# Kernel optimization log

Measured on AMD Instinct MI355X. Metric: run time of the kernel, lower is better.

The kernel has to match this reference:

```python
import jax, jax.numpy as jnp
import numpy as np

PAD = 1
THRESH = 10.0


def setup_inputs() -> dict:
    key = jax.random.key(0)
    k1, k2, k3 = jax.random.split(key, 3)
    x = jax.random.normal(k1, (8, 16, 62, 62), dtype=jnp.float32)
    W = jax.random.normal(k2, (32, 16, 3, 3), dtype=jnp.float32)
    b = jax.random.normal(k3, (32,), dtype=jnp.float32)
    return {"x": x, "W": W, "b": b}


def reference(x, W, b):
    # ZeroPad2d(padding) on all four sides
    x = jnp.pad(x, ((0, 0), (0, 0), (PAD, PAD), (PAD, PAD)))
    T, C, xr, xc = x.shape
    O, _, wr, wc = W.shape
    L = xr * xc

    # get_xfft_thresh: 1D FFT over flattened HxW, zero coeffs with |Re| < thresh
    xf = jnp.fft.fft(x.reshape(T, C, L))                      # (T,C,L) complex
    xf = jnp.where(jnp.abs(xf.real) < THRESH, jnp.zeros_like(xf), xf)

    # get_Wfft: zero-pad kernel to (xr,xc) bottom/right, flatten, reverse along
    # length (flipud(flip([0,1])) nets to a flip of the last axis only), then FFT
    Wp = jnp.pad(W, ((0, 0), (0, 0), (0, xr - wr), (0, xc - wc))).reshape(O, C, L)
    Wf = jnp.fft.fft(Wp[:, :, ::-1])                          # (O,C,L) complex

    # fftConv1D, batched over (image, out_channel):
    y = jnp.fft.ifft(xf[:, None, :, :] * Wf[None, :, :, :]).real  # (T,O,C,L)
    # torch.roll(y, 1) with no dims rolls the FLATTENED (C*L) tensor by 1
    y = jnp.roll(y.reshape(T, O, C * L), 1, axis=-1).reshape(T, O, C, xr, xc)
    y = y.sum(axis=2)                                         # sum over in-channels
    ans_r, ans_c = xr - wr + 1, xc - wc + 1
    y = y[:, :, :ans_r, :ans_c]
    return y + b[None, :, None, None]
```

## Files before the change

kernel.cpp:

```cpp
#include <hip/hip_runtime.h>
#include <math.h>

#define TWO_PI 6.28318530717958647692f
#define NT     512
#define RPW    8
#define PITCH  65
#define THRESH 10.0f
#define C64    0.995184726672196886f
#define S64    0.098017140329560602f
#define C4096  0.999998823451701879f
#define S4096  0.001533980186284766f

__device__ __forceinline__ int brev6(int x) {
    return (int)(__brev((unsigned)x) >> 26);
}

__device__ __forceinline__ void fft64_dif(float (&re)[RPW], float (&im)[RPW],
                                          int lane, float sign) {
    #pragma unroll
    for (int h = 32; h >= 1; h >>= 1) {
        int j = lane & (h - 1);
        float ang = sign * (TWO_PI / 64.0f) * (float)(j * (32 / h));
        float wr, wi;
        __sincosf(ang, &wi, &wr);
        bool upper = (lane & h) != 0;
        float cwr = upper ? wr : 1.0f;
        float cwi = upper ? wi : 0.0f;
        float sgn = upper ? -1.0f : 1.0f;
        #pragma unroll
        for (int m = 0; m < RPW; ++m) {
            float orr = __shfl_xor(re[m], h, 64);
            float oii = __shfl_xor(im[m], h, 64);
            float ar = fmaf(sgn, re[m], orr);
            float ai = fmaf(sgn, im[m], oii);
            re[m] = ar * cwr - ai * cwi;
            im[m] = ar * cwi + ai * cwr;
        }
    }
}

__device__ __forceinline__ void fft64_dit(float (&re)[RPW], float (&im)[RPW],
                                          int lane, float sign) {
    #pragma unroll
    for (int h = 1; h <= 32; h <<= 1) {
        int j = lane & (h - 1);
        float ang = sign * (TWO_PI / 64.0f) * (float)(j * (32 / h));
        float wr, wi;
        __sincosf(ang, &wi, &wr);
        bool upper = (lane & h) != 0;
        float cwr = upper ? wr : 1.0f;
        float cwi = upper ? wi : 0.0f;
        float sgn = upper ? -1.0f : 1.0f;
        #pragma unroll
        for (int m = 0; m < RPW; ++m) {
            float tr = re[m] * cwr - im[m] * cwi;
            float ti = re[m] * cwi + im[m] * cwr;
            float orr = __shfl_xor(tr, h, 64);
            float oii = __shfl_xor(ti, h, 64);
            re[m] = fmaf(sgn, tr, orr);
            im[m] = fmaf(sgn, ti, oii);
        }
    }
}

__global__ __launch_bounds__(NT) void fwd_kernel(const float* __restrict__ x,
                                                 float2* __restrict__ X) {
    __shared__ float sre[64 * PITCH];
    __shared__ float sim[64 * PITCH];
    const int tc   = blockIdx.x;
    const int tid  = threadIdx.x;
    const int lane = tid & 63;
    const int w    = tid >> 6;
    const float* xrow = x + (size_t)tc * 62 * 62;

    for (int idx = tid; idx < 4096; idx += NT) {
        int r = idx >> 6, s = idx & 63;
        float v = 0.0f;
        if (r >= 1 && r <= 62 && s >= 1 && s <= 62)
            v = xrow[(r - 1) * 62 + (s - 1)];
        sre[r * PITCH + s] = v;
    }
    __syncthreads();

    float re[RPW], im[RPW];
    #pragma unroll
    for (int m = 0; m < RPW; ++m) {
        re[m] = sre[lane * PITCH + (w * RPW + m)];
        im[m] = 0.0f;
    }
    fft64_dif(re, im, lane, -1.0f);
    const int k1 = brev6(lane);
    {
        float cr, ci, sr, si;
        __sincosf(-(TWO_PI / 512.0f) * (float)(k1 * w), &ci, &cr);
        __sincosf(-(TWO_PI / 4096.0f) * (float)k1, &si, &sr);
        #pragma unroll
        for (int m = 0; m < RPW; ++m) {
            float rr = re[m] * cr - im[m] * ci;
            im[m]    = re[m] * ci + im[m] * cr;
            re[m]    = rr;
            float nr = cr * sr - ci * si;
            ci = cr * si + ci * sr; cr = nr;
        }
    }
    __syncthreads();
    #pragma unroll
    for (int m = 0; m < RPW; ++m) {
        int n2 = w * RPW + m;
        sre[k1 * PITCH + n2] = re[m];
        sim[k1 * PITCH + n2] = im[m];
    }
    __syncthreads();
    #pragma unroll
    for (int m = 0; m < RPW; ++m) {
        int row = w * RPW + m;
        re[m] = sre[row * PITCH + lane];
        im[m] = sim[row * PITCH + lane];
    }
    fft64_dif(re, im, lane, -1.0f);
    float2* Xrow = X + (size_t)tc * 4096;
    #pragma unroll
    for (int m = 0; m < RPW; ++m) {
        int row = w * RPW + m;
        float rr = re[m], ii = im[m];
        if (fabsf(rr) < THRESH) { rr = 0.0f; ii = 0.0f; }
        Xrow[row * 64 + lane] = make_float2(rr, ii);
    }
}

__global__ __launch_bounds__(NT, 4) void conv_kernel(const float2* __restrict__ X,
                                                     const float* __restrict__ W,
                                                     const float* __restrict__ b,
                                                     float* __restrict__ out) {
    __shared__ float sre[64 * PITCH];
    __shared__ float sim[64 * PITCH];
    __shared__ __align__(16) float Wsh[16 * 12];
    const int t    = blockIdx.x >> 5;
    const int o    = blockIdx.x & 31;
    const int tid  = threadIdx.x;
    const int lane = tid & 63;
    const int w    = tid >> 6;
    if (tid < 144) {
        int c = tid / 9, q = tid - c * 9;
        Wsh[c * 12 + q] = W[o * 144 + tid];
    }
    __syncthreads();

    const int k2 = brev6(lane);
    float elr, eli;
    __sincosf((TWO_PI / 64.0f) * (float)k2, &eli, &elr);

    float ur[RPW], ui[RPW], vr[RPW], vi[RPW], v2r[RPW], v2i[RPW];
    {
        float cur, cui, cvr, cvi;
        __sincosf((TWO_PI / 8.0f) * (float)w, &cui, &cur);
        __sincosf((TWO_PI / 512.0f) * (float)w, &cvi, &cvr);
        #pragma unroll
        for (int m = 0; m < RPW; ++m) {
            ur[m] = cur; ui[m] = cui;
            float vvr = cvr * elr - cvi * eli;
            float vvi = cvr * eli + cvi * elr;
            vr[m] = vvr; vi[m] = vvi;
            v2r[m] = vvr * vvr - vvi * vvi;
            v2i[m] = 2.0f * vvr * vvi;
            float nur = cur * C64 - cui * S64;
            cui = cur * S64 + cui * C64; cur = nur;
            float nvr = cvr * C4096 - cvi * S4096;
            cvi = cvr * S4096 + cvi * C4096; cvr = nvr;
        }
    }

    float Sr[RPW], Si[RPW];
    #pragma unroll
    for (int m = 0; m < RPW; ++m) { Sr[m] = 0.0f; Si[m] = 0.0f; }

    const float2* Xt = X + (size_t)t * 16 * 4096 + (w * (RPW * 64) + lane);
    #pragma unroll 1
    for (int c = 0; c < 16; ++c) {
        const float4* wp = (const float4*)&Wsh[c * 12];
        float4 wa = wp[0];
        float4 wb = wp[1];
        float  w8 = wp[2].x;
        const float2* xp = Xt + c * 4096;
        #pragma unroll
        for (int m = 0; m < RPW; ++m) {
            float2 xv = xp[m * 64];
            float h0r = fmaf(v2r[m], wa.z, fmaf(vr[m], wa.y, wa.x));
            float h0i = fmaf(v2i[m], wa.z, vi[m] * wa.y);
            float h1r = fmaf(v2r[m], wb.y, fmaf(vr[m], wb.x, wa.w));
            float h1i = fmaf(v2i[m], wb.y, vi[m] * wb.x);
            float h2r = fmaf(v2r[m], w8, fmaf(vr[m], wb.w, wb.z));
            float h2i = fmaf(v2i[m], w8, vi[m] * wb.w);
            float inr = fmaf(ur[m], h2r, fmaf(-ui[m], h2i, h1r));
            float ini = fmaf(ur[m], h2i, fmaf( ui[m], h2r, h1i));
            float Pr  = fmaf(ur[m], inr, fmaf(-ui[m], ini, h0r));
            float Pi  = fmaf(ur[m], ini, fmaf( ui[m], inr, h0i));
            Sr[m] = fmaf(xv.x, Pr, fmaf(-xv.y, Pi, Sr[m]));
            Si[m] = fmaf(xv.x, Pi, fmaf( xv.y, Pr, Si[m]));
        }
    }

    float re[RPW], im[RPW];
    #pragma unroll
    for (int m = 0; m < RPW; ++m) { re[m] = Sr[m]; im[m] = Si[m]; }
    fft64_dit(re, im, lane, +1.0f);
    {
        float cr, ci, sr, si;
        __sincosf((TWO_PI / 512.0f) * (float)(lane * w), &ci, &cr);
        __sincosf((TWO_PI / 4096.0f) * (float)lane, &si, &sr);
        #pragma unroll
        for (int m = 0; m < RPW; ++m) {
            float rr = re[m] * cr - im[m] * ci;
            im[m]    = re[m] * ci + im[m] * cr;
            re[m]    = rr;
            float nr = cr * sr - ci * si;
            ci = cr * si + ci * sr; cr = nr;
        }
    }
    #pragma unroll
    for (int m = 0; m < RPW; ++m) {
        int k1 = w * RPW + m;
        sre[k1 * PITCH + lane] = re[m];
        sim[k1 * PITCH + lane] = im[m];
    }
    __syncthreads();
    #pragma unroll
    for (int m = 0; m < RPW; ++m) {
        int n2 = w * RPW + m;
        re[m] = sre[lane * PITCH + n2];
        im[m] = sim[lane * PITCH + n2];
    }
    fft64_dif(re, im, lane, +1.0f);
    __syncthreads();
    const int n1 = brev6(lane);
    #pragma unroll
    for (int m = 0; m < RPW; ++m) {
        int n2 = w * RPW + m;
        sre[n1 * PITCH + n2] = re[m];
    }
    __syncthreads();
    const float bias = b[o];
    float* orow = out + (size_t)blockIdx.x * 62 * 62;
    for (int idx = tid; idx < 62 * 62; idx += NT) {
        int r = idx / 62, s = idx - r * 62;
        orow[idx] = sre[r * PITCH + s] * (1.0f / 4096.0f) + bias;
    }
}

extern "C" void kernel_launch(void* const* d_in, const int* in_sizes, int n_in,
                              void* d_out, int out_size, void* d_ws, size_t ws_size,
                              hipStream_t stream) {
    const float* x = (const float*)d_in[0];
    const float* W = (const float*)d_in[1];
    const float* b = (const float*)d_in[2];
    float* out = (float*)d_out;
    float2* X = (float2*)d_ws;

    fwd_kernel<<<dim3(128), dim3(NT), 0, stream>>>(x, X);
    conv_kernel<<<dim3(256), dim3(NT), 0, stream>>>(X, W, b, out);
}
```

Baseline: 91.15 us.

## Split forward FFT into two half-sized kernels and pipeline conv channel loads

The forward 4096-point FFT becomes two kernels, each launched with 256 blocks that handle half the data. The intermediate result goes through a global workspace, which doubles block-level parallelism on the GPU. The conv kernel now uses packed 2-float vector math, reads weights directly from global memory instead of staging them in shared memory, and software-prefetches the next channel's spectrum while computing the current one. Launch bounds drop from 4 to 2 waves per EU to allow more registers. The costs are an extra kernel launch, a global round-trip for the intermediate data, and possibly lower occupancy.

```diff
diff --git a/kernel.cpp b/kernel.cpp
--- a/kernel.cpp
+++ b/kernel.cpp
@@ -11,11 +11,20 @@
 #define C4096  0.999998823451701879f
 #define S4096  0.001533980186284766f
 
+typedef float v2f __attribute__((ext_vector_type(2)));
+
 __device__ __forceinline__ int brev6(int x) {
     return (int)(__brev((unsigned)x) >> 26);
 }
 
-__device__ __forceinline__ void fft64_dif(float (&re)[RPW], float (&im)[RPW],
+__device__ __forceinline__ v2f cmul_add(v2f a, v2f b, v2f acc) {
+    acc += (v2f){a.x, a.x} * b;
+    acc += (v2f){a.y, a.y} * (v2f){-b.y, b.x};
+    return acc;
+}
+
+template<int R>
+__device__ __forceinline__ void fft64_dif(float (&re)[R], float (&im)[R],
                                           int lane, float sign) {
     #pragma unroll
     for (int h = 32; h >= 1; h >>= 1) {
@@ -28,7 +37,7 @@
         float cwi = upper ? wi : 0.0f;
         float sgn = upper ? -1.0f : 1.0f;
         #pragma unroll
-        for (int m = 0; m < RPW; ++m) {
+        for (int m = 0; m < R; ++m) {
             float orr = __shfl_xor(re[m], h, 64);
             float oii = __shfl_xor(im[m], h, 64);
             float ar = fmaf(sgn, re[m], orr);
@@ -39,7 +48,8 @@
     }
 }
 
-__device__ __forceinline__ void fft64_dit(float (&re)[RPW], float (&im)[RPW],
+template<int R>
+__device__ __forceinline__ void fft64_dit(float (&re)[R], float (&im)[R],
                                           int lane, float sign) {
     #pragma unroll
     for (int h = 1; h <= 32; h <<= 1) {
@@ -52,7 +62,7 @@
         float cwi = upper ? wi : 0.0f;
         float sgn = upper ? -1.0f : 1.0f;
         #pragma unroll
-        for (int m = 0; m < RPW; ++m) {
+        for (int m = 0; m < R; ++m) {
             float tr = re[m] * cwr - im[m] * cwi;
             float ti = re[m] * cwi + im[m] * cwr;
             float orr = __shfl_xor(tr, h, 64);
@@ -63,37 +73,159 @@
     }
 }
 
-__global__ __launch_bounds__(NT) void fwd_kernel(const float* __restrict__ x,
-                                                 float2* __restrict__ X) {
-    __shared__ float sre[64 * PITCH];
-    __shared__ float sim[64 * PITCH];
-    const int tc   = blockIdx.x;
+__global__ __launch_bounds__(NT) void fwdA_kernel(const float* __restrict__ x,
+                                                  float2* __restrict__ Xa) {
+    __shared__ float sre[64 * 33];
+    __shared__ float sim[64 * 33];
+    const int task = blockIdx.x >> 1;
+    const int h    = blockIdx.x & 1;
     const int tid  = threadIdx.x;
     const int lane = tid & 63;
     const int w    = tid >> 6;
-    const float* xrow = x + (size_t)tc * 62 * 62;
-
-    for (int idx = tid; idx < 4096; idx += NT) {
-        int r = idx >> 6, s = idx & 63;
+    const float* xr = x + (size_t)task * 62 * 62;
+    for (int idx = tid; idx < 64 * 32; idx += NT) {
+        int r = idx >> 5, j = idx & 31;
+        int n2 = 32 * h + j;
         float v = 0.0f;
-        if (r >= 1 && r <= 62 && s >= 1 && s <= 62)
-            v = xrow[(r - 1) * 62 + (s - 1)];
-        sre[r * PITCH + s] = v;
-    }
-    __syncthreads();
+        if (r >= 1 && r <= 62 && n2 >= 1 && n2 <= 62)
+            v = xr[(r - 1) * 62 + (n2 - 1)];
+        sre[r * 33 + j] = v;
+    }
+    __syncthreads();
+    float re[4], im[4];
+    #pragma unroll
+    for (int m = 0; m < 4; ++m) {
+        re[m] = sre[lane * 33 + (w * 4 + m)];
+        im[m] = 0.0f;
+    }
+    fft64_dif<4>(re, im, lane, -1.0f);
+    __syncthreads();
+    const int k1 = brev6(lane);
+    #pragma unroll
+    for (int m = 0; m < 4; ++m) {
+        int j  = w * 4 + m;
+        int n2 = 32 * h + j;
+        float cr, ci;
+        __sincosf(-(TWO_PI / 4096.0f) * (float)(k1 * n2), &ci, &cr);
+        sre[k1 * 33 + j] = re[m] * cr - im[m] * ci;
+        sim[k1 * 33 + j] = re[m] * ci + im[m] * cr;
+    }
+    __syncthreads();
+    float2* Arow = Xa + (size_t)task * 4096;
+    for (int idx = tid; idx < 64 * 32; idx += NT) {
+        int k = idx >> 5, j = idx & 31;
+        Arow[k * 64 + 32 * h + j] = make_float2(sre[k * 33 + j], sim[k * 33 + j]);
+    }
+}
+
+__global__ __launch_bounds__(NT) void fwdB_kernel(const float2* __restrict__ Xa,
+                                                  float2* __restrict__ X) {
+    const int task = blockIdx.x >> 1;
+    const int h    = blockIdx.x & 1;
+    const int tid  = threadIdx.x;
+    const int lane = tid & 63;
+    const int w    = tid >> 6;
+    const float2* Arow = Xa + (size_t)task * 4096;
+    float re[4], im[4];
+    #pragma unroll
+    for (int m = 0; m < 4; ++m) {
+        float2 xv = Arow[(32 * h + w * 4 + m) * 64 + lane];
+        re[m] = xv.x; im[m] = xv.y;
+    }
+    fft64_dif<4>(re, im, lane, -1.0f);
+    float2* Xrow = X + (size_t)task * 4096;
+    #pragma unroll
+    for (int m = 0; m < 4; ++m) {
+        float rr = re[m], ii = im[m];
+        if (fabsf(rr) < THRESH) { rr = 0.0f; ii = 0.0f; }
+        Xrow[(32 * h + w * 4 + m) * 64 + lane] = make_float2(rr, ii);
+    }
+}
+
+__global__ __launch_bounds__(NT, 2) void conv_kernel(const float2* __restrict__ X,
+                                                     const float* __restrict__ W,
+                                                     const float* __restrict__ b,
+                                                     float* __restrict__ out) {
+    __shared__ float sre[64 * PITCH];
+    __shared__ float sim[64 * PITCH];
+    const int t    = blockIdx.x >> 5;
+    const int o    = blockIdx.x & 31;
+    const int tid  = threadIdx.x;
+    const int lane = tid & 63;
+    const int w    = tid >> 6;
+
+    const int k2 = brev6(lane);
+    float elr, eli;
+    __sincosf((TWO_PI / 64.0f) * (float)k2, &eli, &elr);
+
+    v2f uv[RPW], vv[RPW], v2v[RPW];
+    {
+        float cur, cui, cvr, cvi;
+        __sincosf((TWO_PI / 8.0f) * (float)w, &cui, &cur);
+        __sincosf((TWO_PI / 512.0f) * (float)w, &cvi, &cvr);
+        #pragma unroll
+        for (int m = 0; m < RPW; ++m) {
+            uv[m] = (v2f){cur, cui};
+            float vvr = cvr * elr - cvi * eli;
+            float vvi = cvr * eli + cvi * elr;
+            vv[m]  = (v2f){vvr, vvi};
+            v2v[m] = (v2f){vvr * vvr - vvi * vvi, 2.0f * vvr * vvi};
+            float nur = cur * C64 - cui * S64;
+            cui = cur * S64 + cui * C64; cur = nur;
+            float nvr = cvr * C4096 - cvi * S4096;
+            cvi = cvr * S4096 + cvi * C4096; cvr = nvr;
+        }
+    }
+
+    v2f S[RPW];
+    #pragma unroll
+    for (int m = 0; m < RPW; ++m) S[m] = (v2f){0.0f, 0.0f};
+
+    const float2* Xt = X + (size_t)t * 16 * 4096 + (w * (RPW * 64) + lane);
+    const float*  wo = W + o * 144;
+
+    v2f xb[RPW];
+    #pragma unroll
+    for (int m = 0; m < RPW; ++m) {
+        float2 q = Xt[m * 64];
+        xb[m] = (v2f){q.x, q.y};
+    }
+    #pragma unroll 1
+    for (int c = 0; c < 16; ++c) {
+        v2f xn[RPW];
+        if (c < 15) {
+            const float2* xp = Xt + (c + 1) * 4096;
+            #pragma unroll
+            for (int m = 0; m < RPW; ++m) {
+                float2 q = xp[m * 64];
+                xn[m] = (v2f){q.x, q.y};
+            }
+        }
+        const float wa0 = wo[c*9+0], wa1 = wo[c*9+1], wa2 = wo[c*9+2];
+        const float wa3 = wo[c*9+3], wa4 = wo[c*9+4], wa5 = wo[c*9+5];
+        const float wa6 = wo[c*9+6], wa7 = wo[c*9+7], wa8 = wo[c*9+8];
+        #pragma unroll
+        for (int m = 0; m < RPW; ++m) {
+            v2f v = vv[m], v2 = v2v[m], u = uv[m];
+            v2f h0 = (v2f){wa0, 0.0f}; h0 += v * wa1; h0 += v2 * wa2;
+            v2f h1 = (v2f){wa3, 0.0f}; h1 += v * wa4; h1 += v2 * wa5;
+            v2f h2 = (v2f){wa6, 0.0f}; h2 += v * wa7; h2 += v2 * wa8;
+            v2f in = cmul_add(u, h2, h1);
+            v2f P  = cmul_add(u, in, h0);
+            S[m]   = cmul_add(xb[m], P, S[m]);
+        }
+        #pragma unroll
+        for (int m = 0; m < RPW; ++m) xb[m] = xn[m];
+    }
 
     float re[RPW], im[RPW];
     #pragma unroll
-    for (int m = 0; m < RPW; ++m) {
-        re[m] = sre[lane * PITCH + (w * RPW + m)];
-        im[m] = 0.0f;
-    }
-    fft64_dif(re, im, lane, -1.0f);
-    const int k1 = brev6(lane);
+    for (int m = 0; m < RPW; ++m) { re[m] = S[m].x; im[m] = S[m].y; }
+    fft64_dit<RPW>(re, im, lane, +1.0f);
     {
         float cr, ci, sr, si;
-        __sincosf(-(TWO_PI / 512.0f) * (float)(k1 * w), &ci, &cr);
-        __sincosf(-(TWO_PI / 4096.0f) * (float)k1, &si, &sr);
+        __sincosf((TWO_PI / 512.0f) * (float)(lane * w), &ci, &cr);
+        __sincosf((TWO_PI / 4096.0f) * (float)lane, &si, &sr);
         #pragma unroll
         for (int m = 0; m < RPW; ++m) {
             float rr = re[m] * cr - im[m] * ci;
@@ -103,120 +235,6 @@
             ci = cr * si + ci * sr; cr = nr;
         }
     }
-    __syncthreads();
-    #pragma unroll
-    for (int m = 0; m < RPW; ++m) {
-        int n2 = w * RPW + m;
-        sre[k1 * PITCH + n2] = re[m];
-        sim[k1 * PITCH + n2] = im[m];
-    }
-    __syncthreads();
-    #pragma unroll
-    for (int m = 0; m < RPW; ++m) {
-        int row = w * RPW + m;
-        re[m] = sre[row * PITCH + lane];
-        im[m] = sim[row * PITCH + lane];
-    }
-    fft64_dif(re, im, lane, -1.0f);
-    float2* Xrow = X + (size_t)tc * 4096;
-    #pragma unroll
-    for (int m = 0; m < RPW; ++m) {
-        int row = w * RPW + m;
-        float rr = re[m], ii = im[m];
-        if (fabsf(rr) < THRESH) { rr = 0.0f; ii = 0.0f; }
-        Xrow[row * 64 + lane] = make_float2(rr, ii);
-    }
-}
-
-__global__ __launch_bounds__(NT, 4) void conv_kernel(const float2* __restrict__ X,
-                                                     const float* __restrict__ W,
-                                                     const float* __restrict__ b,
-                                                     float* __restrict__ out) {
-    __shared__ float sre[64 * PITCH];
-    __shared__ float sim[64 * PITCH];
-    __shared__ __align__(16) float Wsh[16 * 12];
-    const int t    = blockIdx.x >> 5;
-    const int o    = blockIdx.x & 31;
-    const int tid  = threadIdx.x;
-    const int lane = tid & 63;
-    const int w    = tid >> 6;
-    if (tid < 144) {
-        int c = tid / 9, q = tid - c * 9;
-        Wsh[c * 12 + q] = W[o * 144 + tid];
-    }
-    __syncthreads();
-
-    const int k2 = brev6(lane);
-    float elr, eli;
-    __sincosf((TWO_PI / 64.0f) * (float)k2, &eli, &elr);
-
-    float ur[RPW], ui[RPW], vr[RPW], vi[RPW], v2r[RPW], v2i[RPW];
-    {
-        float cur, cui, cvr, cvi;
-        __sincosf((TWO_PI / 8.0f) * (float)w, &cui, &cur);
-        __sincosf((TWO_PI / 512.0f) * (float)w, &cvi, &cvr);
-        #pragma unroll
-        for (int m = 0; m < RPW; ++m) {
-            ur[m] = cur; ui[m] = cui;
-            float vvr = cvr * elr - cvi * eli;
-            float vvi = cvr * eli + cvi * elr;
-            vr[m] = vvr; vi[m] = vvi;
-            v2r[m] = vvr * vvr - vvi * vvi;
-            v2i[m] = 2.0f * vvr * vvi;
-            float nur = cur * C64 - cui * S64;
-            cui = cur * S64 + cui * C64; cur = nur;
-            float nvr = cvr * C4096 - cvi * S4096;
-            cvi = cvr * S4096 + cvi * C4096; cvr = nvr;
-        }
-    }
-
-    float Sr[RPW], Si[RPW];
-    #pragma unroll
-    for (int m = 0; m < RPW; ++m) { Sr[m] = 0.0f; Si[m] = 0.0f; }
-
-    const float2* Xt = X + (size_t)t * 16 * 4096 + (w * (RPW * 64) + lane);
-    #pragma unroll 1
-    for (int c = 0; c < 16; ++c) {
-        const float4* wp = (const float4*)&Wsh[c * 12];
-        float4 wa = wp[0];
-        float4 wb = wp[1];
-        float  w8 = wp[2].x;
-        const float2* xp = Xt + c * 4096;
-        #pragma unroll
-        for (int m = 0; m < RPW; ++m) {
-            float2 xv = xp[m * 64];
-            float h0r = fmaf(v2r[m], wa.z, fmaf(vr[m], wa.y, wa.x));
-            float h0i = fmaf(v2i[m], wa.z, vi[m] * wa.y);
-            float h1r = fmaf(v2r[m], wb.y, fmaf(vr[m], wb.x, wa.w));
-            float h1i = fmaf(v2i[m], wb.y, vi[m] * wb.x);
-            float h2r = fmaf(v2r[m], w8, fmaf(vr[m], wb.w, wb.z));
-            float h2i = fmaf(v2i[m], w8, vi[m] * wb.w);
-            float inr = fmaf(ur[m], h2r, fmaf(-ui[m], h2i, h1r));
-            float ini = fmaf(ur[m], h2i, fmaf( ui[m], h2r, h1i));
-            float Pr  = fmaf(ur[m], inr, fmaf(-ui[m], ini, h0r));
-            float Pi  = fmaf(ur[m], ini, fmaf( ui[m], inr, h0i));
-            Sr[m] = fmaf(xv.x, Pr, fmaf(-xv.y, Pi, Sr[m]));
-            Si[m] = fmaf(xv.x, Pi, fmaf( xv.y, Pr, Si[m]));
-        }
-    }
-
-    float re[RPW], im[RPW];
-    #pragma unroll
-    for (int m = 0; m < RPW; ++m) { re[m] = Sr[m]; im[m] = Si[m]; }
-    fft64_dit(re, im, lane, +1.0f);
-    {
-        float cr, ci, sr, si;
-        __sincosf((TWO_PI / 512.0f) * (float)(lane * w), &ci, &cr);
-        __sincosf((TWO_PI / 4096.0f) * (float)lane, &si, &sr);
-        #pragma unroll
-        for (int m = 0; m < RPW; ++m) {
-            float rr = re[m] * cr - im[m] * ci;
-            im[m]    = re[m] * ci + im[m] * cr;
-            re[m]    = rr;
-            float nr = cr * sr - ci * si;
-            ci = cr * si + ci * sr; cr = nr;
-        }
-    }
     #pragma unroll
     for (int m = 0; m < RPW; ++m) {
         int k1 = w * RPW + m;
@@ -230,7 +248,7 @@
         re[m] = sre[lane * PITCH + n2];
         im[m] = sim[lane * PITCH + n2];
     }
-    fft64_dif(re, im, lane, +1.0f);
+    fft64_dif<RPW>(re, im, lane, +1.0f);
     __syncthreads();
     const int n1 = brev6(lane);
     #pragma unroll
@@ -254,8 +272,10 @@
     const float* W = (const float*)d_in[1];
     const float* b = (const float*)d_in[2];
     float* out = (float*)d_out;
-    float2* X = (float2*)d_ws;
-
-    fwd_kernel<<<dim3(128), dim3(NT), 0, stream>>>(x, X);
+    float2* Xa = (float2*)d_ws;
+    float2* X  = Xa + 128 * 4096;
+
+    fwdA_kernel<<<dim3(256), dim3(NT), 0, stream>>>(x, Xa);
+    fwdB_kernel<<<dim3(256), dim3(NT), 0, stream>>>(Xa, X);
     conv_kernel<<<dim3(256), dim3(NT), 0, stream>>>(X, W, b, out);
 }
```

Result: faster. 87.84 us (-3.6%).
